# Kernel optimization log

Hardware: AMD Instinct MI355X
Metric: run time of the kernel (lower is better)

## Reference

```python
import jax, jax.numpy as jnp
import numpy as np

K = 5          # number of neighbors (init kwarg k)
EPS = 1e-7     # init kwarg eps
_D2_MIN = 1e-12  # clamp squared distances so sqrt is grad-safe on the diagonal


def _cdist(A):
    # Euclidean pairwise distances, [N, N]
    sq = jnp.sum(A * A, axis=1)
    d2 = sq[:, None] + sq[None, :] - 2.0 * (A @ A.T)
    return jnp.sqrt(jnp.maximum(d2, _D2_MIN))


def setup_inputs() -> dict:
    key = jax.random.key(0)
    k1, k2 = jax.random.split(key)
    X = jax.random.normal(k1, (8192, 512), dtype=jnp.float32)
    Z = jax.random.normal(k2, (8192, 128), dtype=jnp.float32)
    return {"X": X, "Z": Z}


def reference(X, Z):
    # 0.98-quantile of row norms (torch.quantile default = linear interpolation)
    normA1 = jnp.quantile(jnp.sqrt(jnp.sum(X ** 2, axis=1)), 0.98)
    normA2 = jnp.quantile(jnp.sqrt(jnp.sum(Z ** 2, axis=1)), 0.98)

    # --- neighbor mask + LID on X ---
    x_dist = (_cdist(X) + EPS) / normA1                      # [N, N]
    neg_vals, idx = jax.lax.top_k(-x_dist, K + 1)            # k+1 smallest, ascending
    values = -neg_vals[:, 1:]                                # drop self, [N, K]
    nn_mask = idx[:, 1:]                                     # neighbor indices, [N, K]
    lid_X = jnp.sum(jnp.log10(values) - jnp.log10(values[:, -1:]), axis=1)  # [N]

    # --- gather same neighbors in Z-space ---
    z_dist = (_cdist(Z) + EPS) / normA2                      # [N, N]
    extracted = jnp.take_along_axis(z_dist, nn_mask, axis=1)  # [N, K]
    norm_v = jnp.max(extracted, axis=1, keepdims=True)        # [N, 1]
    lid_Z = jnp.sum(jnp.log10(extracted) - jnp.log10(norm_v), axis=1)  # [N]

    N = X.shape[0]
    diff = K / (lid_X + EPS) - K / (lid_Z + EPS)
    return jnp.sum(jnp.square(diff)) / (N * K * K)
```

## Files before the change

kernel.cpp:

```cpp
#include <hip/hip_runtime.h>
#include <hip/hip_bf16.h>
#include <math.h>


#define NROWS 8192
#define DX 512
#define DZ 128
#define KNN 5
#define NSTRIP 4
#define SSPAN (NROWS / NSTRIP)
#define BM 128
#define BN 256
#define NJT (SSPAN / BN)
#define NSTEPS (NJT * 8)
#define NCAND (NSTRIP * KNN)
#define CAP 64
#define QSCALE 30.0f

typedef int i32x4 __attribute__((ext_vector_type(4)));
typedef int i32x16 __attribute__((ext_vector_type(16)));

__device__ __forceinline__ bool ilexless(int d1, int i1, int d2, int i2) {
  return (d1 < d2) || (d1 == d2 && i1 < i2);
}
__device__ __forceinline__ bool flexless(float d1, int i1, float d2, int i2) {
  return (d1 < d2) || (d1 == d2 && i1 < i2);
}

__device__ __forceinline__ void ins5k(int k, int* md) {
  if (k >= md[4]) return;
  int nk = k;
#pragma unroll
  for (int p = 0; p < 5; ++p) {
    const bool sw = nk < md[p];
    const int tk = sw ? md[p] : nk;
    md[p] = sw ? nk : md[p];
    nk = tk;
  }
}
__device__ __forceinline__ void ins8i(int d, int i, int* md, int* mi) {
  if (!ilexless(d, i, md[7], mi[7])) return;
  int nd = d, ni = i;
#pragma unroll
  for (int p = 0; p < 8; ++p) {
    const bool sw = ilexless(nd, ni, md[p], mi[p]);
    const int td = sw ? md[p] : nd; const int ti = sw ? mi[p] : ni;
    md[p] = sw ? nd : md[p]; mi[p] = sw ? ni : mi[p];
    nd = td; ni = ti;
  }
}
__device__ __forceinline__ void ins5f(float d, int i, float* md, int* mi) {
  if (!flexless(d, i, md[4], mi[4])) return;
  float nd = d; int ni = i;
#pragma unroll
  for (int p = 0; p < 5; ++p) {
    const bool sw = flexless(nd, ni, md[p], mi[p]);
    const float td = sw ? md[p] : nd; const int ti = sw ? mi[p] : ni;
    md[p] = sw ? nd : md[p]; mi[p] = sw ? ni : mi[p];
    nd = td; ni = ti;
  }
}

__device__ __forceinline__ void gload_lds16(const void* g, void* l) {
  __builtin_amdgcn_global_load_lds((const __attribute__((address_space(1))) void*)g,
                                   (__attribute__((address_space(3))) void*)l,
                                   16, 0, 0);
}

__global__ __launch_bounds__(256) void cvtsq_kernel(const float* __restrict__ X,
                                                    signed char* __restrict__ Xq,
                                                    float* __restrict__ sqx,
                                                    int* __restrict__ sqq) {
  const int w = threadIdx.x >> 6;
  const int lane = threadIdx.x & 63;
  const int row = (blockIdx.x << 2) + w;
  const float* p = X + (size_t)row * DX + lane * 8;
  const float4 v0 = *(const float4*)(p);
  const float4 v1 = *(const float4*)(p + 4);
  float xs[8] = {v0.x, v0.y, v0.z, v0.w, v1.x, v1.y, v1.z, v1.w};
  float s = 0.f;
  int q[8];
  int si = 0;
#pragma unroll
  for (int j = 0; j < 8; ++j) {
    s = fmaf(xs[j], xs[j], s);
    q[j] = (int)rintf(fminf(fmaxf(xs[j] * QSCALE, -127.f), 127.f));
    si += q[j] * q[j];
  }
  const int b0 = (q[0] & 255) | ((q[1] & 255) << 8) | ((q[2] & 255) << 16) | ((q[3] & 255) << 24);
  const int b1 = (q[4] & 255) | ((q[5] & 255) << 8) | ((q[6] & 255) << 16) | ((q[7] & 255) << 24);
  *(int2*)(Xq + (size_t)row * DX + lane * 8) = make_int2(b0, b1);
#pragma unroll
  for (int off = 32; off > 0; off >>= 1) {
    s += __shfl_down(s, off, 64);
    si += __shfl_down(si, off, 64);
  }
  if (lane == 0) { sqx[row] = s; sqq[row] = si; }
}

__global__ __launch_bounds__(1024) void stats_kernel(const int* __restrict__ sqq,
                                                     float* __restrict__ stats) {
  __shared__ double sw[16], sw2[16];
  const int t = threadIdx.x;
  double s = 0.0, s2 = 0.0;
  for (int i = t; i < NROWS; i += 1024) {
    const double v = (double)sqq[i];
    s += v; s2 += v * v;
  }
#pragma unroll
  for (int off = 32; off > 0; off >>= 1) {
    s += __shfl_down(s, off, 64);
    s2 += __shfl_down(s2, off, 64);
  }
  if ((t & 63) == 0) { sw[t >> 6] = s; sw2[t >> 6] = s2; }
  __syncthreads();
  if (t < 16) {
    double v = sw[t], v2 = sw2[t];
#pragma unroll
    for (int off = 8; off > 0; off >>= 1) {
      v += __shfl_down(v, off, 64);
      v2 += __shfl_down(v2, off, 64);
    }
    if (t == 0) {
      const double mu = v / (double)NROWS;
      stats[0] = (float)mu;
      stats[1] = (float)(v2 / (double)NROWS - mu * mu);
    }
  }
}

__global__ __launch_bounds__(256) void row_sq_kernel(const float* __restrict__ A,
                                                     float* __restrict__ out, int cols) {
  const int w = threadIdx.x >> 6;
  const int lane = threadIdx.x & 63;
  const int row = (blockIdx.x << 2) + w;
  const float* p = A + (size_t)row * cols;
  float s = 0.f;
  for (int c = lane; c < cols; c += 64) { float v = p[c]; s = fmaf(v, v, s); }
#pragma unroll
  for (int off = 32; off > 0; off >>= 1) s += __shfl_down(s, off, 64);
  if (lane == 0) out[row] = s;
}

__global__ __launch_bounds__(512, 2) void knn_i8_kernel(const signed char* __restrict__ Xq,
                                                        const int* __restrict__ sqq,
                                                        const float* __restrict__ stats,
                                                        int* __restrict__ cand_i,
                                                        int* __restrict__ cand_m) {
  extern __shared__ __align__(16) char lds[];
  char* ldsA = lds;
  char* ldsB = lds + 65536;
  int* sbf = (int*)(lds + 114688);
  int* cnt = (int*)(lds + 147456);

  const int bid = blockIdx.x;
  const int strip = bid & 3;
  const int rowchunk = bid >> 2;
  const int I0 = rowchunk * BM;
  const int J0 = strip * SSPAN;

  const int t = threadIdx.x;
  const int w = t >> 6;
  const int lane = t & 63;
  const int l31 = lane & 31, lh5 = lane >> 5;
  const int cq = w & 3, rh = w >> 2;

  if (t < BM) cnt[t] = 0;

  const float mu = stats[0];
  const float var = stats[1];
  const int r0 = I0 + rh * 64 + l31;
  const int tau0 = (int)(mu - 2.2f * sqrtf(var + (mu * 0.0078125f) * (float)sqq[r0]));
  const int tau1 = (int)(mu - 2.2f * sqrtf(var + (mu * 0.0078125f) * (float)sqq[r0 + 32]));

#pragma unroll
  for (int i = 0; i < 8; ++i) {
    const int idx = w * 8 + i;
    const int g = idx >> 1, half = idx & 1;
    gload_lds16(Xq + (size_t)(I0 + half * 64 + lane) * DX + (g << 4),
                ldsA + g * 2048 + half * 1024);
  }
  auto STAGE_B = [&](int buf, int s) {
    const int jt = s >> 3, kb = s & 7;
#pragma unroll
    for (int j = 0; j < 2; ++j) {
      const int idx = w * 2 + j;
      const int g = idx >> 2, c4 = idx & 3;
      gload_lds16(Xq + (size_t)(J0 + jt * BN + c4 * 64 + lane) * DX + (kb << 6) + (g << 4),
                  ldsB + buf * 16384 + g * 4096 + c4 * 1024);
    }
  };
  STAGE_B(0, 0);
  STAGE_B(1, 1);

  const i32x16 z16 = {0, 0, 0, 0, 0, 0, 0, 0, 0, 0, 0, 0, 0, 0, 0, 0};
  i32x16 acc[2][2];

  for (int s = 0; s < NSTEPS; ++s) {
    if (s < NSTEPS - 1) {
      asm volatile("s_waitcnt vmcnt(2)" ::: "memory");
    } else {
      asm volatile("s_waitcnt vmcnt(0)" ::: "memory");
    }
    __builtin_amdgcn_s_barrier();
    __builtin_amdgcn_sched_barrier(0);
    if (s + 2 < NSTEPS) STAGE_B((s + 2) % 3, s + 2);

    const int kb = s & 7, jt = s >> 3;
    if (kb == 0) { acc[0][0] = z16; acc[0][1] = z16; acc[1][0] = z16; acc[1][1] = z16; }
    const char* bB = ldsB + (s % 3) * 16384;
    const int rbase = rh << 10;
#pragma unroll
    for (int ktl = 0; ktl < 2; ++ktl) {
      const int gB = (ktl << 1) | lh5;
      const int gA = (kb << 2) | gB;
      const i32x4 ap0 = *(const i32x4*)(bB + gB * 4096 + ((cq * 64 + l31) << 4));
      const i32x4 ap1 = *(const i32x4*)(bB + gB * 4096 + ((cq * 64 + 32 + l31) << 4));
      const i32x4 bp0 = *(const i32x4*)(ldsA + gA * 2048 + rbase + (l31 << 4));
      const i32x4 bp1 = *(const i32x4*)(ldsA + gA * 2048 + rbase + ((32 + l31) << 4));
      acc[0][0] = __builtin_amdgcn_mfma_i32_32x32x32_i8(ap0, bp0, acc[0][0], 0, 0, 0);
      acc[0][1] = __builtin_amdgcn_mfma_i32_32x32x32_i8(ap0, bp1, acc[0][1], 0, 0, 0);
      acc[1][0] = __builtin_amdgcn_mfma_i32_32x32x32_i8(ap1, bp0, acc[1][0], 0, 0, 0);
      acc[1][1] = __builtin_amdgcn_mfma_i32_32x32x32_i8(ap1, bp1, acc[1][1], 0, 0, 0);
    }
    if (kb == 7) {
#pragma unroll
      for (int n = 0; n < 2; ++n) {
        const int colb = J0 + jt * BN + cq * 64 + n * 32;
        const int* qp = sqq + colb + (lh5 << 2);
        const i32x4 q0 = *(const i32x4*)(qp);
        const i32x4 q1 = *(const i32x4*)(qp + 8);
        const i32x4 q2 = *(const i32x4*)(qp + 16);
        const i32x4 q3 = *(const i32x4*)(qp + 24);
#pragma unroll
        for (int m = 0; m < 2; ++m) {
          const int lr = rh * 64 + m * 32 + l31;
          const int tau = m ? tau1 : tau0;
#pragma unroll
          for (int reg = 0; reg < 16; ++reg) {
            const int qv = (reg < 4) ? q0[reg & 3] : (reg < 8) ? q1[reg & 3]
                         : (reg < 12) ? q2[reg & 3] : q3[reg & 3];
            const int d = qv - 2 * acc[n][m][reg];
            if (d < tau) {
              const int creg = (reg & 3) + ((reg >> 2) << 3) + (lh5 << 2);
              const int col = colb + creg;
              const int slot = atomicAdd(&cnt[lr], 1);
              if (slot < CAP) {
                int v = d - (tau - 262144);
                v = max(v, 0);
                sbf[lr * CAP + slot] = (v << 13) | col;
              }
            }
          }
        }
      }
    }
  }

  __syncthreads();

  int* pm = (int*)ldsB;
  {
    const int row = t >> 2, sub = t & 3;
    const int rg = I0 + row;
    int md[5];
#pragma unroll
    for (int q = 0; q < 5; ++q) md[q] = 0x7fffffff;
    const int c = min(cnt[row], CAP);
    for (int s2 = sub; s2 < c; s2 += 4) {
      const int key = sbf[row * CAP + s2];
      if ((key & 8191) != rg) ins5k(key, md);
    }
#pragma unroll
    for (int q = 0; q < 5; ++q) pm[(row * 4 + sub) * 5 + q] = md[q];
  }
  __syncthreads();
  if (t < BM) {
    int md[5];
#pragma unroll
    for (int q = 0; q < 5; ++q) md[q] = 0x7fffffff;
    for (int c = 0; c < 4; ++c)
#pragma unroll
      for (int q = 0; q < 5; ++q) ins5k(pm[(t * 4 + c) * 5 + q], md);
    const size_t base = (size_t)(I0 + t) * NCAND + strip * KNN;
#pragma unroll
    for (int q = 0; q < 5; ++q) {
      cand_m[base + q] = md[q];
      cand_i[base + q] = (md[q] == 0x7fffffff) ? 0x7fffffff : (md[q] & 8191);
    }
  }
}

__global__ __launch_bounds__(256) void rerank_kernel(const float* __restrict__ X,
                                                     const float* __restrict__ Z,
                                                     const float* __restrict__ sqx,
                                                     const float* __restrict__ sqz,
                                                     const int* __restrict__ cand_i,
                                                     const int* __restrict__ cand_m,
                                                     float* __restrict__ row_out) {
  __shared__ float xrow[4][DX];
  const int w = threadIdx.x >> 6;
  const int lane = threadIdx.x & 63;
  const int row = (blockIdx.x << 2) + w;

  const float* xp = X + (size_t)row * DX + lane * 8;
  *(float4*)&xrow[w][lane * 8] = *(const float4*)(xp);
  *(float4*)&xrow[w][lane * 8 + 4] = *(const float4*)(xp + 4);

  int cm = 0x7fffffff, ci = 0x7fffffff;
  if (lane < NCAND) {
    cm = cand_m[(size_t)row * NCAND + lane];
    ci = cand_i[(size_t)row * NCAND + lane];
  }
  __syncthreads();

  int m8[8], i8v[8];
#pragma unroll
  for (int q = 0; q < 8; ++q) { m8[q] = 0x7fffffff; i8v[q] = 0x7fffffff; }
#pragma unroll
  for (int c = 0; c < NCAND; ++c) {
    const int dm = __shfl(cm, c, 64);
    const int di = __shfl(ci, c, 64);
    ins8i(dm, di, m8, i8v);
  }

  const int cgrp = lane >> 3, sgi = lane & 7;
  int j = (cgrp == 0) ? i8v[0] : (cgrp == 1) ? i8v[1] : (cgrp == 2) ? i8v[2] :
          (cgrp == 3) ? i8v[3] : (cgrp == 4) ? i8v[4] : (cgrp == 5) ? i8v[5] :
          (cgrp == 6) ? i8v[6] : i8v[7];
  if ((unsigned)j >= NROWS) j = 0;
  const float* yp = X + (size_t)j * DX + sgi * 64;
  const float* xq_ = &xrow[w][sgi * 64];
  float dot = 0.f;
#pragma unroll 8
  for (int k = 0; k < 64; k += 4) {
    const float4 xv = *(const float4*)(xq_ + k);
    const float4 yv = *(const float4*)(yp + k);
    dot = fmaf(xv.x, yv.x, dot);
    dot = fmaf(xv.y, yv.y, dot);
    dot = fmaf(xv.z, yv.z, dot);
    dot = fmaf(xv.w, yv.w, dot);
  }
  dot += __shfl_xor(dot, 1, 64);
  dot += __shfl_xor(dot, 2, 64);
  dot += __shfl_xor(dot, 4, 64);
  const float d2 = sqx[row] + sqx[j] - 2.f * dot;

  float fd[5]; int fi[5];
#pragma unroll
  for (int q = 0; q < 5; ++q) { fd[q] = INFINITY; fi[q] = 0x7fffffff; }
#pragma unroll
  for (int cc = 0; cc < 8; ++cc) {
    const float dd = __shfl(d2, cc * 8, 64);
    if (lane == 0) ins5f(dd, i8v[cc], fd, fi);
  }
  float lidX = 0.f;
  if (lane == 0) {
    const float v4 = sqrtf(fmaxf(fd[4], 1e-12f)) + 1e-7f;
    const float l4 = log10f(v4);
#pragma unroll
    for (int q = 0; q < 5; ++q) {
      const float v = sqrtf(fmaxf(fd[q], 1e-12f)) + 1e-7f;
      lidX += log10f(v) - l4;
    }
  }
  int nb[5];
#pragma unroll
  for (int q = 0; q < 5; ++q) {
    nb[q] = __shfl(fi[q], 0, 64);
    if ((unsigned)nb[q] >= NROWS) nb[q] = 0;
  }

  const float zi0 = Z[(size_t)row * DZ + lane];
  const float zi1 = Z[(size_t)row * DZ + 64 + lane];
  float ez[5];
#pragma unroll
  for (int q = 0; q < 5; ++q) {
    const float* zn = Z + (size_t)nb[q] * DZ;
    float p = fmaf(zi0, zn[lane], zi1 * zn[64 + lane]);
#pragma unroll
    for (int off = 32; off > 0; off >>= 1) p += __shfl_down(p, off, 64);
    ez[q] = p;
  }
  if (lane == 0) {
    const float sqzr = sqz[row];
    float e[5];
    float mx = -INFINITY;
#pragma unroll
    for (int q = 0; q < 5; ++q) {
      const float d2z = sqzr + sqz[nb[q]] - 2.f * ez[q];
      e[q] = sqrtf(fmaxf(d2z, 1e-12f)) + 1e-7f;
      mx = fmaxf(mx, e[q]);
    }
    const float lmx = log10f(mx);
    float lidZ = 0.f;
#pragma unroll
    for (int q = 0; q < 5; ++q) lidZ += log10f(e[q]) - lmx;
    const float diff = 5.0f / (lidX + 1e-7f) - 5.0f / (lidZ + 1e-7f);
    row_out[row] = diff * diff;
  }
}

__global__ __launch_bounds__(1024) void reduce_kernel(const float* __restrict__ row_out,
                                                      float* __restrict__ out) {
  __shared__ float sw[16];
  const int t = threadIdx.x;
  float s = 0.f;
  for (int i = t; i < NROWS; i += 1024) s += row_out[i];
#pragma unroll
  for (int off = 32; off > 0; off >>= 1) s += __shfl_down(s, off, 64);
  if ((t & 63) == 0) sw[t >> 6] = s;
  __syncthreads();
  if (t < 16) {
    float v = sw[t];
#pragma unroll
    for (int off = 8; off > 0; off >>= 1) v += __shfl_down(v, off, 64);
    if (t == 0) out[0] = v * (1.0f / (8192.0f * 25.0f));
  }
}

extern "C" void kernel_launch(void* const* d_in, const int* in_sizes, int n_in,
                              void* d_out, int out_size, void* d_ws, size_t ws_size,
                              hipStream_t stream) {
  const float* X = (const float*)d_in[0];
  const float* Z = (const float*)d_in[1];
  float* out = (float*)d_out;

  char* wb = (char*)d_ws;
  signed char* Xq = (signed char*)wb;
  float* sqx = (float*)(wb + (size_t)NROWS * DX);
  int* sqq = (int*)(sqx + NROWS);
  float* sqz = (float*)(sqq + NROWS);
  int* cand_i = (int*)(sqz + NROWS);
  int* cand_m = cand_i + (size_t)NROWS * NCAND;
  float* row_out = (float*)(cand_m + (size_t)NROWS * NCAND);
  float* stats = row_out + NROWS;

  cvtsq_kernel<<<NROWS / 4, 256, 0, stream>>>(X, Xq, sqx, sqq);
  stats_kernel<<<1, 1024, 0, stream>>>(sqq, stats);
  row_sq_kernel<<<NROWS / 4, 256, 0, stream>>>(Z, sqz, DZ);
  knn_i8_kernel<<<NSTRIP * (NROWS / BM), 512, 147968, stream>>>(Xq, sqq, stats, cand_i, cand_m);
  rerank_kernel<<<NROWS / 4, 256, 0, stream>>>(X, Z, sqx, sqz, cand_i, cand_m, row_out);
  reduce_kernel<<<1, 1024, 0, stream>>>(row_out, out);
}
```

Measured before the change: 128.1 us.

## Use 1024-thread KNN blocks, stage column norms in LDS, fold stats into cvtsq

Doubles the KNN block to 1024 threads, so each wave computes a 32x64 tile with half the accumulators instead of 64x64, and one block occupies a CU instead of two. Column squared norms are staged into LDS rather than read from global memory during filtering, and candidate merging uses 8 sub-threads per row. The separate stats kernel is removed: mean and variance sums are now accumulated with 64-bit atomics in cvtsq after a memset. This trades one launch and some register pressure for heavier global atomics and a different occupancy and latency-hiding profile.

```diff
diff --git a/kernel.cpp b/kernel.cpp
--- a/kernel.cpp
+++ b/kernel.cpp
@@ -70,7 +70,8 @@
 __global__ __launch_bounds__(256) void cvtsq_kernel(const float* __restrict__ X,
                                                     signed char* __restrict__ Xq,
                                                     float* __restrict__ sqx,
-                                                    int* __restrict__ sqq) {
+                                                    int* __restrict__ sqq,
+                                                    unsigned long long* __restrict__ ssum) {
   const int w = threadIdx.x >> 6;
   const int lane = threadIdx.x & 63;
   const int row = (blockIdx.x << 2) + w;
@@ -95,37 +96,10 @@
     s += __shfl_down(s, off, 64);
     si += __shfl_down(si, off, 64);
   }
-  if (lane == 0) { sqx[row] = s; sqq[row] = si; }
-}
-
-__global__ __launch_bounds__(1024) void stats_kernel(const int* __restrict__ sqq,
-                                                     float* __restrict__ stats) {
-  __shared__ double sw[16], sw2[16];
-  const int t = threadIdx.x;
-  double s = 0.0, s2 = 0.0;
-  for (int i = t; i < NROWS; i += 1024) {
-    const double v = (double)sqq[i];
-    s += v; s2 += v * v;
-  }
-#pragma unroll
-  for (int off = 32; off > 0; off >>= 1) {
-    s += __shfl_down(s, off, 64);
-    s2 += __shfl_down(s2, off, 64);
-  }
-  if ((t & 63) == 0) { sw[t >> 6] = s; sw2[t >> 6] = s2; }
-  __syncthreads();
-  if (t < 16) {
-    double v = sw[t], v2 = sw2[t];
-#pragma unroll
-    for (int off = 8; off > 0; off >>= 1) {
-      v += __shfl_down(v, off, 64);
-      v2 += __shfl_down(v2, off, 64);
-    }
-    if (t == 0) {
-      const double mu = v / (double)NROWS;
-      stats[0] = (float)mu;
-      stats[1] = (float)(v2 / (double)NROWS - mu * mu);
-    }
+  if (lane == 0) {
+    sqx[row] = s; sqq[row] = si;
+    atomicAdd(&ssum[0], (unsigned long long)(unsigned)si);
+    atomicAdd(&ssum[1], (unsigned long long)(unsigned)si * (unsigned long long)(unsigned)si);
   }
 }
 
@@ -142,16 +116,17 @@
   if (lane == 0) out[row] = s;
 }
 
-__global__ __launch_bounds__(512, 2) void knn_i8_kernel(const signed char* __restrict__ Xq,
-                                                        const int* __restrict__ sqq,
-                                                        const float* __restrict__ stats,
-                                                        int* __restrict__ cand_i,
-                                                        int* __restrict__ cand_m) {
+__global__ __launch_bounds__(1024, 1) void knn_i8_kernel(const signed char* __restrict__ Xq,
+                                                         const int* __restrict__ sqq,
+                                                         const unsigned long long* __restrict__ ssum,
+                                                         int* __restrict__ cand_i,
+                                                         int* __restrict__ cand_m) {
   extern __shared__ __align__(16) char lds[];
   char* ldsA = lds;
   char* ldsB = lds + 65536;
-  int* sbf = (int*)(lds + 114688);
-  int* cnt = (int*)(lds + 147456);
+  int* qs = (int*)(lds + 114688);
+  int* sbf = (int*)(lds + 122880);
+  int* cnt = (int*)(lds + 155648);
 
   const int bid = blockIdx.x;
   const int strip = bid & 3;
@@ -167,38 +142,40 @@
 
   if (t < BM) cnt[t] = 0;
 
-  const float mu = stats[0];
-  const float var = stats[1];
-  const int r0 = I0 + rh * 64 + l31;
-  const int tau0 = (int)(mu - 2.2f * sqrtf(var + (mu * 0.0078125f) * (float)sqq[r0]));
-  const int tau1 = (int)(mu - 2.2f * sqrtf(var + (mu * 0.0078125f) * (float)sqq[r0 + 32]));
-
-#pragma unroll
-  for (int i = 0; i < 8; ++i) {
-    const int idx = w * 8 + i;
+  const double S1 = (double)ssum[0];
+  const double S2 = (double)ssum[1];
+  const double mud = S1 * (1.0 / 8192.0);
+  const float mu = (float)mud;
+  const float var = (float)(S2 * (1.0 / 8192.0) - mud * mud);
+  const int lr = (rh << 5) + l31;
+  const int rg = I0 + lr;
+  const int tau = (int)(mu - 2.2f * sqrtf(var + (mu * 0.0078125f) * (float)sqq[rg]));
+
+#pragma unroll
+  for (int i = 0; i < 4; ++i) {
+    const int idx = (w << 2) + i;
     const int g = idx >> 1, half = idx & 1;
     gload_lds16(Xq + (size_t)(I0 + half * 64 + lane) * DX + (g << 4),
                 ldsA + g * 2048 + half * 1024);
   }
+  if (w < 8)
+    gload_lds16((const char*)(sqq + J0) + (w << 10) + (lane << 4),
+                (char*)qs + (w << 10));
   auto STAGE_B = [&](int buf, int s) {
     const int jt = s >> 3, kb = s & 7;
-#pragma unroll
-    for (int j = 0; j < 2; ++j) {
-      const int idx = w * 2 + j;
-      const int g = idx >> 2, c4 = idx & 3;
-      gload_lds16(Xq + (size_t)(J0 + jt * BN + c4 * 64 + lane) * DX + (kb << 6) + (g << 4),
-                  ldsB + buf * 16384 + g * 4096 + c4 * 1024);
-    }
+    const int g = w >> 2, c4 = w & 3;
+    gload_lds16(Xq + (size_t)(J0 + jt * BN + c4 * 64 + lane) * DX + (kb << 6) + (g << 4),
+                ldsB + buf * 16384 + g * 4096 + c4 * 1024);
   };
   STAGE_B(0, 0);
   STAGE_B(1, 1);
 
   const i32x16 z16 = {0, 0, 0, 0, 0, 0, 0, 0, 0, 0, 0, 0, 0, 0, 0, 0};
-  i32x16 acc[2][2];
+  i32x16 acc[2];
 
   for (int s = 0; s < NSTEPS; ++s) {
     if (s < NSTEPS - 1) {
-      asm volatile("s_waitcnt vmcnt(2)" ::: "memory");
+      asm volatile("s_waitcnt vmcnt(1)" ::: "memory");
     } else {
       asm volatile("s_waitcnt vmcnt(0)" ::: "memory");
     }
@@ -207,49 +184,40 @@
     if (s + 2 < NSTEPS) STAGE_B((s + 2) % 3, s + 2);
 
     const int kb = s & 7, jt = s >> 3;
-    if (kb == 0) { acc[0][0] = z16; acc[0][1] = z16; acc[1][0] = z16; acc[1][1] = z16; }
+    if (kb == 0) { acc[0] = z16; acc[1] = z16; }
     const char* bB = ldsB + (s % 3) * 16384;
-    const int rbase = rh << 10;
 #pragma unroll
     for (int ktl = 0; ktl < 2; ++ktl) {
       const int gB = (ktl << 1) | lh5;
       const int gA = (kb << 2) | gB;
       const i32x4 ap0 = *(const i32x4*)(bB + gB * 4096 + ((cq * 64 + l31) << 4));
       const i32x4 ap1 = *(const i32x4*)(bB + gB * 4096 + ((cq * 64 + 32 + l31) << 4));
-      const i32x4 bp0 = *(const i32x4*)(ldsA + gA * 2048 + rbase + (l31 << 4));
-      const i32x4 bp1 = *(const i32x4*)(ldsA + gA * 2048 + rbase + ((32 + l31) << 4));
-      acc[0][0] = __builtin_amdgcn_mfma_i32_32x32x32_i8(ap0, bp0, acc[0][0], 0, 0, 0);
-      acc[0][1] = __builtin_amdgcn_mfma_i32_32x32x32_i8(ap0, bp1, acc[0][1], 0, 0, 0);
-      acc[1][0] = __builtin_amdgcn_mfma_i32_32x32x32_i8(ap1, bp0, acc[1][0], 0, 0, 0);
-      acc[1][1] = __builtin_amdgcn_mfma_i32_32x32x32_i8(ap1, bp1, acc[1][1], 0, 0, 0);
+      const i32x4 bp = *(const i32x4*)(ldsA + gA * 2048 + (((rh << 5) + l31) << 4));
+      acc[0] = __builtin_amdgcn_mfma_i32_32x32x32_i8(ap0, bp, acc[0], 0, 0, 0);
+      acc[1] = __builtin_amdgcn_mfma_i32_32x32x32_i8(ap1, bp, acc[1], 0, 0, 0);
     }
     if (kb == 7) {
 #pragma unroll
       for (int n = 0; n < 2; ++n) {
         const int colb = J0 + jt * BN + cq * 64 + n * 32;
-        const int* qp = sqq + colb + (lh5 << 2);
+        const int* qp = qs + jt * BN + cq * 64 + n * 32 + (lh5 << 2);
         const i32x4 q0 = *(const i32x4*)(qp);
         const i32x4 q1 = *(const i32x4*)(qp + 8);
         const i32x4 q2 = *(const i32x4*)(qp + 16);
         const i32x4 q3 = *(const i32x4*)(qp + 24);
 #pragma unroll
-        for (int m = 0; m < 2; ++m) {
-          const int lr = rh * 64 + m * 32 + l31;
-          const int tau = m ? tau1 : tau0;
-#pragma unroll
-          for (int reg = 0; reg < 16; ++reg) {
-            const int qv = (reg < 4) ? q0[reg & 3] : (reg < 8) ? q1[reg & 3]
-                         : (reg < 12) ? q2[reg & 3] : q3[reg & 3];
-            const int d = qv - 2 * acc[n][m][reg];
-            if (d < tau) {
-              const int creg = (reg & 3) + ((reg >> 2) << 3) + (lh5 << 2);
-              const int col = colb + creg;
-              const int slot = atomicAdd(&cnt[lr], 1);
-              if (slot < CAP) {
-                int v = d - (tau - 262144);
-                v = max(v, 0);
-                sbf[lr * CAP + slot] = (v << 13) | col;
-              }
+        for (int reg = 0; reg < 16; ++reg) {
+          const int qv = (reg < 4) ? q0[reg & 3] : (reg < 8) ? q1[reg & 3]
+                       : (reg < 12) ? q2[reg & 3] : q3[reg & 3];
+          const int d = qv - 2 * acc[n][reg];
+          if (d < tau) {
+            const int creg = (reg & 3) + ((reg >> 2) << 3) + (lh5 << 2);
+            const int col = colb + creg;
+            const int slot = atomicAdd(&cnt[lr], 1);
+            if (slot < CAP) {
+              int v = d - (tau - 262144);
+              v = max(v, 0);
+              sbf[lr * CAP + slot] = (v << 13) | col;
             }
           }
         }
@@ -261,27 +229,27 @@
 
   int* pm = (int*)ldsB;
   {
-    const int row = t >> 2, sub = t & 3;
-    const int rg = I0 + row;
+    const int row = t >> 3, sub = t & 7;
+    const int rgg = I0 + row;
     int md[5];
 #pragma unroll
     for (int q = 0; q < 5; ++q) md[q] = 0x7fffffff;
     const int c = min(cnt[row], CAP);
-    for (int s2 = sub; s2 < c; s2 += 4) {
+    for (int s2 = sub; s2 < c; s2 += 8) {
       const int key = sbf[row * CAP + s2];
-      if ((key & 8191) != rg) ins5k(key, md);
-    }
-#pragma unroll
-    for (int q = 0; q < 5; ++q) pm[(row * 4 + sub) * 5 + q] = md[q];
+      if ((key & 8191) != rgg) ins5k(key, md);
+    }
+#pragma unroll
+    for (int q = 0; q < 5; ++q) pm[(row * 8 + sub) * 5 + q] = md[q];
   }
   __syncthreads();
   if (t < BM) {
     int md[5];
 #pragma unroll
     for (int q = 0; q < 5; ++q) md[q] = 0x7fffffff;
-    for (int c = 0; c < 4; ++c)
-#pragma unroll
-      for (int q = 0; q < 5; ++q) ins5k(pm[(t * 4 + c) * 5 + q], md);
+    for (int c = 0; c < 8; ++c)
+#pragma unroll
+      for (int q = 0; q < 5; ++q) ins5k(pm[(t * 8 + c) * 5 + q], md);
     const size_t base = (size_t)(I0 + t) * NCAND + strip * KNN;
 #pragma unroll
     for (int q = 0; q < 5; ++q) {
@@ -434,12 +402,12 @@
   int* cand_i = (int*)(sqz + NROWS);
   int* cand_m = cand_i + (size_t)NROWS * NCAND;
   float* row_out = (float*)(cand_m + (size_t)NROWS * NCAND);
-  float* stats = row_out + NROWS;
-
-  cvtsq_kernel<<<NROWS / 4, 256, 0, stream>>>(X, Xq, sqx, sqq);
-  stats_kernel<<<1, 1024, 0, stream>>>(sqq, stats);
+  unsigned long long* ssum = (unsigned long long*)(row_out + NROWS);
+
+  hipMemsetAsync(ssum, 0, 16, stream);
+  cvtsq_kernel<<<NROWS / 4, 256, 0, stream>>>(X, Xq, sqx, sqq, ssum);
   row_sq_kernel<<<NROWS / 4, 256, 0, stream>>>(Z, sqz, DZ);
-  knn_i8_kernel<<<NSTRIP * (NROWS / BM), 512, 147968, stream>>>(Xq, sqq, stats, cand_i, cand_m);
+  knn_i8_kernel<<<NSTRIP * (NROWS / BM), 1024, 156160, stream>>>(Xq, sqq, ssum, cand_i, cand_m);
   rerank_kernel<<<NROWS / 4, 256, 0, stream>>>(X, Z, sqx, sqz, cand_i, cand_m, row_out);
   reduce_kernel<<<1, 1024, 0, stream>>>(row_out, out);
 }
```

Measured after the change: 314.6 us. 146% more time.
